# Kernel optimization log

Hardware: AMD Instinct MI355X
Metric: run time of the kernel (lower is better)

Reference implementation:

```python
import jax, jax.numpy as jnp
import numpy as np

B, S, D, H = 2, 2048, 1024, 16
DK = D // H  # 64
SCALE = DK ** (-0.5)  # NOTE: module divides by this, i.e. multiplies scores by sqrt(DK)


def setup_inputs() -> dict:
    key = jax.random.key(0)
    ks = jax.random.split(key, 9)
    std = D ** (-0.5)
    return {
        "x": jax.random.normal(ks[0], (B, S, D), dtype=jnp.float32),
        "attention_mask": jnp.ones((B, S), dtype=jnp.int32),
        "Wq": jax.random.normal(ks[1], (D, D), dtype=jnp.float32) * std,
        "bq": jnp.zeros((D,), dtype=jnp.float32),
        "Wk": jax.random.normal(ks[2], (D, D), dtype=jnp.float32) * std,
        "bk": jnp.zeros((D,), dtype=jnp.float32),
        "Wv": jax.random.normal(ks[3], (D, D), dtype=jnp.float32) * std,
        "bv": jnp.zeros((D,), dtype=jnp.float32),
        "Wo": jax.random.normal(ks[4], (D, D), dtype=jnp.float32) * std,
        "bo": jnp.zeros((D,), dtype=jnp.float32),
    }


def _split_heads(t):
    # [B, S, D] -> [B, H, S, DK]
    return t.reshape(B, S, H, DK).transpose(0, 2, 1, 3)


def reference(x, attention_mask, Wq, bq, Wk, bk, Wv, bv, Wo, bo):
    q = _split_heads(x @ Wq.T + bq)
    k = _split_heads(x @ Wk.T + bk)
    v = _split_heads(x @ Wv.T + bv)

    # faithful to source: sim = (q @ k^T) / scale with scale = dk**-0.5
    sim = jnp.einsum("bhqd,bhkd->bhqk", q, k) / SCALE

    # key-padding mask: positions where attention_mask == 0 are masked out
    neg = jnp.finfo(sim.dtype).min
    keep = attention_mask.astype(bool)[:, None, None, :]  # [B,1,1,S]
    sim = jnp.where(keep, sim, neg)

    attn = jax.nn.softmax(sim, axis=-1)  # dropout is identity at inference
    out = jnp.einsum("bhqk,bhkd->bhqd", attn, v)
    out = out.transpose(0, 2, 1, 3).reshape(B, S, D)  # merge heads
    return out @ Wo.T + bo
```

## Files before the change

kernel.cpp:

```cpp
#include <hip/hip_runtime.h>
#include <hip/hip_bf16.h>
#include <math.h>

#define BB 2
#define SS 2048
#define DD 1024
#define HH 16
#define DKK 64
#define BH (BB * HH)

typedef __bf16 bf16_t;
typedef _Float16 f16_t;
typedef __attribute__((ext_vector_type(8))) _Float16 f16x8;
typedef __attribute__((ext_vector_type(4))) _Float16 f16x4;
typedef __attribute__((ext_vector_type(4))) float f32x4;

#define GLD_LDS(gp, lp) __builtin_amdgcn_global_load_lds( \
    (const __attribute__((address_space(1))) void*)(gp),  \
    (__attribute__((address_space(3))) void*)(lp), 16, 0, 0)

__global__ void cast_x_flags(const float* __restrict__ in, f16_t* __restrict__ out,
                             const int* __restrict__ mask, int* __restrict__ flags, int n) {
    int i = blockIdx.x * blockDim.x + threadIdx.x;
    int stride = gridDim.x * blockDim.x;
    for (; i < n; i += stride) out[i] = (f16_t)in[i];
    if (blockIdx.x == 0 && threadIdx.x < BB * (SS / 128)) {
        int f = threadIdx.x;
        int b = f / (SS / 128), t = f % (SS / 128);
        const int* p = mask + b * SS + t * 128;
        int all = 1;
        for (int j = 0; j < 128; ++j) all &= (p[j] != 0);
        flags[f] = all;
    }
}

__global__ void cast_wqk(const float* __restrict__ Wq, const float* __restrict__ Wk,
                         f16_t* __restrict__ hi, f16_t* __restrict__ lo, int nw) {
    int i = blockIdx.x * blockDim.x + threadIdx.x;
    int stride = gridDim.x * blockDim.x;
    for (; i < 2 * nw; i += stride) {
        float v = (i < nw) ? Wq[i] : Wk[i - nw];
        f16_t h = (f16_t)v;
        hi[i] = h;
        lo[i] = (f16_t)(v - (float)h);
    }
}

__global__ void cast_wvo(const float* __restrict__ Wv, const float* __restrict__ Wo,
                         f16_t* __restrict__ wv, f16_t* __restrict__ wo, int nw) {
    int i = blockIdx.x * blockDim.x + threadIdx.x;
    int stride = gridDim.x * blockDim.x;
    for (; i < 2 * nw; i += stride) {
        if (i < nw) wv[i] = (f16_t)Wv[i];
        else        wo[i - nw] = (f16_t)Wo[i - nw];
    }
}

__global__ __launch_bounds__(256) void gemm_qkv(const f16_t* __restrict__ Af,
                                                const f16_t* __restrict__ Wqkh,
                                                const f16_t* __restrict__ Wqkl,
                                                const f16_t* __restrict__ Wvf,
                                                const float* __restrict__ bq,
                                                const float* __restrict__ bk,
                                                const float* __restrict__ bv,
                                                f16_t* __restrict__ q_o,
                                                f16_t* __restrict__ k_o,
                                                f16_t* __restrict__ vt_o,
                                                int K) {
    __shared__ __align__(16) f16_t sA[4096];
    __shared__ __align__(16) f16_t sB0[4096];
    __shared__ __align__(16) f16_t sB1[4096];

    const int tid  = threadIdx.x;
    const int wv   = tid >> 6;
    const int lane = tid & 63;
    const int quad = lane >> 4;
    const int l15  = lane & 15;
    const int wr   = wv >> 1;
    const int wc   = wv & 1;
    const int row0 = blockIdx.y * 128;
    const int col0 = blockIdx.x * 128;
    const bool isV = (col0 >= 2048);

    const f16_t* B0 = isV ? (Wvf + (long)(col0 - 2048) * K) : (Wqkh + (long)col0 * K);
    const f16_t* B1 = isV ? nullptr : (Wqkl + (long)col0 * K);

    f32x4 acc[4][4] = {};

    const int srow = tid >> 2;
    const int scol = (tid & 3) * 8;
    const long aoff = (long)(row0 + srow) * K + scol;
    const long boff = (long)srow * K + scol;

    if (isV) {
#pragma unroll 1
        for (int kb = 0; kb < K; kb += 32) {
#pragma unroll
            for (int p = 0; p < 2; ++p) {
                const long go = (long)p * 64 * K + kb;
                const int lo = p * 2048 + wv * 512;
                GLD_LDS(Af + aoff + go, sA + lo);
                GLD_LDS(B0 + boff + go, sB0 + lo);
            }
            __syncthreads();
            f16x8 af[4];
#pragma unroll
            for (int mt = 0; mt < 4; ++mt)
                af[mt] = *(const f16x8*)&sA[(wr * 64 + mt * 16 + l15) * 32 + quad * 8];
#pragma unroll
            for (int nt = 0; nt < 4; ++nt) {
                f16x8 b0 = *(const f16x8*)&sB0[(wc * 64 + nt * 16 + l15) * 32 + quad * 8];
#pragma unroll
                for (int mt = 0; mt < 4; ++mt)
                    acc[mt][nt] = __builtin_amdgcn_mfma_f32_16x16x32_f16(af[mt], b0, acc[mt][nt], 0, 0, 0);
            }
            __syncthreads();
        }
    } else {
#pragma unroll 1
        for (int kb = 0; kb < K; kb += 32) {
#pragma unroll
            for (int p = 0; p < 2; ++p) {
                const long go = (long)p * 64 * K + kb;
                const int lo = p * 2048 + wv * 512;
                GLD_LDS(Af + aoff + go, sA + lo);
                GLD_LDS(B0 + boff + go, sB0 + lo);
                GLD_LDS(B1 + boff + go, sB1 + lo);
            }
            __syncthreads();
            f16x8 af[4];
#pragma unroll
            for (int mt = 0; mt < 4; ++mt)
                af[mt] = *(const f16x8*)&sA[(wr * 64 + mt * 16 + l15) * 32 + quad * 8];
#pragma unroll
            for (int nt = 0; nt < 4; ++nt) {
                f16x8 b0 = *(const f16x8*)&sB0[(wc * 64 + nt * 16 + l15) * 32 + quad * 8];
                f16x8 b1 = *(const f16x8*)&sB1[(wc * 64 + nt * 16 + l15) * 32 + quad * 8];
#pragma unroll
                for (int mt = 0; mt < 4; ++mt) {
                    acc[mt][nt] = __builtin_amdgcn_mfma_f32_16x16x32_f16(af[mt], b0, acc[mt][nt], 0, 0, 0);
                    acc[mt][nt] = __builtin_amdgcn_mfma_f32_16x16x32_f16(af[mt], b1, acc[mt][nt], 0, 0, 0);
                }
            }
            __syncthreads();
        }
    }

    if (isV) {
#pragma unroll
        for (int nt = 0; nt < 4; ++nt) {
            const int colv = (col0 - 2048) + wc * 64 + nt * 16 + l15;
            const float bvv = bv[colv];
            const int hq = colv >> 6, dk = colv & 63;
#pragma unroll
            for (int mt = 0; mt < 4; ++mt) {
                const int grow0 = row0 + wr * 64 + mt * 16 + quad * 4;
                const int bq2 = grow0 >> 11;
                const int s0  = grow0 & (SS - 1);
                f16x4 pk;
#pragma unroll
                for (int r = 0; r < 4; ++r) pk[r] = (f16_t)(acc[mt][nt][r] + bvv);
                *(f16x4*)(vt_o + ((long)(bq2 * HH + hq) * DKK + dk) * SS + s0) = pk;
            }
        }
    } else {
        const bool isK = (col0 >= 1024);
        const float* bias = isK ? bk : bq;
        f16_t* op = isK ? k_o : q_o;
#pragma unroll
        for (int nt = 0; nt < 4; ++nt) {
            const int gcol = (col0 & 1023) + wc * 64 + nt * 16 + l15;
            const float bvv = bias[gcol];
            const int hq = gcol >> 6, dk = gcol & 63;
#pragma unroll
            for (int mt = 0; mt < 4; ++mt) {
                const int grow0 = row0 + wr * 64 + mt * 16 + quad * 4;
#pragma unroll
                for (int r = 0; r < 4; ++r) {
                    int grow = grow0 + r;
                    float vvv = acc[mt][nt][r] + bvv;
                    long off = (((long)(grow >> 11) * HH + hq) * SS + (grow & (SS - 1))) * DKK + dk;
                    op[off] = (f16_t)vvv;
                }
            }
        }
    }
}

__global__ __launch_bounds__(256) void gemm_o(const f16_t* __restrict__ Ah,
                                              const f16_t* __restrict__ Bhp,
                                              const float* __restrict__ bias,
                                              float* __restrict__ outf,
                                              int N, int K) {
    __shared__ __align__(16) f16_t lds[2048 + 4096];
    f16_t* Ash = lds;
    f16_t* Bsh = lds + 2048;

    const int tid  = threadIdx.x;
    const int wv   = tid >> 6;
    const int lane = tid & 63;
    const int quad = lane >> 4;
    const int l15  = lane & 15;
    const int wr   = wv >> 1;
    const int wc   = wv & 1;
    const int row0 = blockIdx.y * 64;
    const int col0 = blockIdx.x * 128;

    f32x4 acc[2][4] = {};

    const int srow = lane >> 2;
    const int scol = (lane & 3) * 8;
    const f16_t* gA  = Ah  + (long)(row0 + wv * 16 + srow) * K + scol;
    const f16_t* gB0 = Bhp + (long)(col0 + wv * 16 + srow) * K + scol;
    const f16_t* gB1 = Bhp + (long)(col0 + (wv + 4) * 16 + srow) * K + scol;
    f16_t* lA  = Ash + wv * 512;
    f16_t* lB0 = Bsh + wv * 512;
    f16_t* lB1 = Bsh + (wv + 4) * 512;

#pragma unroll 1
    for (int kb = 0; kb < K; kb += 32) {
        GLD_LDS(gA + kb, lA);
        GLD_LDS(gB0 + kb, lB0);
        GLD_LDS(gB1 + kb, lB1);
        __syncthreads();

        f16x8 af[2];
#pragma unroll
        for (int mt = 0; mt < 2; ++mt)
            af[mt] = *(const f16x8*)&Ash[(wr * 32 + mt * 16 + l15) * 32 + quad * 8];
#pragma unroll
        for (int nt = 0; nt < 4; ++nt) {
            f16x8 bh = *(const f16x8*)&Bsh[(wc * 64 + nt * 16 + l15) * 32 + quad * 8];
#pragma unroll
            for (int mt = 0; mt < 2; ++mt)
                acc[mt][nt] = __builtin_amdgcn_mfma_f32_16x16x32_f16(af[mt], bh, acc[mt][nt], 0, 0, 0);
        }
        __syncthreads();
    }

#pragma unroll
    for (int mt = 0; mt < 2; ++mt) {
#pragma unroll
        for (int nt = 0; nt < 4; ++nt) {
            const int gcol  = col0 + wc * 64 + nt * 16 + l15;
            const float bvv = bias[gcol];
            const int grow0 = row0 + wr * 32 + mt * 16 + quad * 4;
#pragma unroll
            for (int r = 0; r < 4; ++r)
                outf[(long)(grow0 + r) * N + gcol] = acc[mt][nt][r] + bvv;
        }
    }
}

__global__ __launch_bounds__(256) void attn_mfma5(const f16_t* __restrict__ Qp,
                                                  const f16_t* __restrict__ Kp,
                                                  const f16_t* __restrict__ Vtp,
                                                  const int* __restrict__ mask,
                                                  const int* __restrict__ flags,
                                                  f16_t* __restrict__ ctx,
                                                  int seq_len) {
    __shared__ __align__(16) f16_t Ksh[2][4096];
    __shared__ __align__(16) f16_t Vsh[2][4096];
    __shared__ __align__(16) f16_t Psh[4][16 * 132];

    const int tid  = threadIdx.x;
    const int wv   = tid >> 6;
    const int lane = tid & 63;
    const int quad = lane >> 4;
    const int l15  = lane & 15;
    const int bh   = blockIdx.y;
    const int b    = bh >> 4;
    const int h    = bh & 15;
    const int q0   = blockIdx.x * 64 + wv * 16;

    const long kb = (long)bh * SS * DKK;

    f16x8 qf[2];
    {
        const f16_t* pq = Qp + kb + (long)(q0 + l15) * DKK + quad * 8;
        qf[0] = *(const f16x8*)pq;
        qf[1] = *(const f16x8*)(pq + 32);
        const f16_t qs = (f16_t)(8.0f * 1.44269504088896f);
#pragma unroll
        for (int j = 0; j < 8; ++j) { qf[0][j] *= qs; qf[1][j] *= qs; }
    }

    f16x8 ones;
#pragma unroll
    for (int j = 0; j < 8; ++j) ones[j] = (f16_t)1.0f;

    f32x4 o[4], lacc;
    float m[4];
#pragma unroll
    for (int r = 0; r < 4; ++r) {
        o[r] = (f32x4){0.f, 0.f, 0.f, 0.f};
        m[r] = -1e30f;
    }
    lacc = (f32x4){0.f, 0.f, 0.f, 0.f};

    const int* mrow = mask + b * SS;
    const int* frow = flags + b * (SS / 128);

    const int srow8 = lane >> 3;
    const int gcolB = ((lane & 7) ^ srow8) * 8;

#pragma unroll 1
    for (int kt = 0; kt < seq_len; kt += 128) {
#pragma unroll
        for (int c = 0; c < 2; ++c) {
            const int kc = kt + c * 64;
#pragma unroll
            for (int p = 0; p < 2; ++p) {
                const int i = wv * 2 + p;
                const int row = i * 8 + srow8;
                GLD_LDS(Kp + kb + (long)(kc + row) * DKK + gcolB, &Ksh[c][i * 512]);
                GLD_LDS(Vtp + kb + (long)row * SS + kc + gcolB, &Vsh[c][i * 512]);
            }
        }
        __syncthreads();

        f32x4 s[8];
#pragma unroll
        for (int nt = 0; nt < 8; ++nt) s[nt] = (f32x4){0.f, 0.f, 0.f, 0.f};
#pragma unroll
        for (int nt = 0; nt < 8; ++nt) {
            const int c = nt >> 2;
            const int kr = (nt & 3) * 16 + l15;
#pragma unroll
            for (int dt = 0; dt < 2; ++dt) {
                f16x8 kf = *(const f16x8*)&Ksh[c][kr * 64 + (((dt * 4 + quad) ^ (l15 & 7)) << 3)];
                s[nt] = __builtin_amdgcn_mfma_f32_16x16x32_f16(qf[dt], kf, s[nt], 0, 0, 0);
            }
        }

        if (!frow[kt >> 7]) {
#pragma unroll
            for (int nt = 0; nt < 8; ++nt) {
                int keep = mrow[kt + nt * 16 + l15];
#pragma unroll
                for (int r = 0; r < 4; ++r)
                    s[nt][r] = keep ? s[nt][r] : -1e30f;
            }
        }

        float tm[4];
#pragma unroll
        for (int r = 0; r < 4; ++r) {
            tm[r] = fmaxf(fmaxf(fmaxf(s[0][r], s[1][r]), fmaxf(s[2][r], s[3][r])),
                          fmaxf(fmaxf(s[4][r], s[5][r]), fmaxf(s[6][r], s[7][r])));
        }
#pragma unroll
        for (int off = 1; off < 16; off <<= 1) {
#pragma unroll
            for (int r = 0; r < 4; ++r) tm[r] = fmaxf(tm[r], __shfl_xor(tm[r], off));
        }

        float alpha[4];
#pragma unroll
        for (int r = 0; r < 4; ++r) {
            float mn = fmaxf(m[r], tm[r]);
            alpha[r] = exp2f(m[r] - mn);
            m[r] = mn;
        }

#pragma unroll
        for (int nt = 0; nt < 8; ++nt) {
#pragma unroll
            for (int r = 0; r < 4; ++r) {
                float p = exp2f(s[nt][r] - m[r]);
                Psh[wv][(quad * 4 + r) * 132 + nt * 16 + l15] = (f16_t)p;
            }
        }

#pragma unroll
        for (int t = 0; t < 4; ++t)
#pragma unroll
            for (int r = 0; r < 4; ++r) o[t][r] *= alpha[r];
#pragma unroll
        for (int r = 0; r < 4; ++r) lacc[r] *= alpha[r];

#pragma unroll
        for (int kk = 0; kk < 4; ++kk) {
            const int c = kk >> 1;
            const int kk2 = kk & 1;
            f16x4 pa = *(const f16x4*)&Psh[wv][l15 * 132 + kk * 32 + quad * 8];
            f16x4 pb = *(const f16x4*)&Psh[wv][l15 * 132 + kk * 32 + quad * 8 + 4];
            f16x8 pf = __builtin_shufflevector(pa, pb, 0, 1, 2, 3, 4, 5, 6, 7);
#pragma unroll
            for (int t = 0; t < 4; ++t) {
                const int vr = t * 16 + l15;
                f16x8 vf = *(const f16x8*)&Vsh[c][vr * 64 + (((kk2 * 4 + quad) ^ (l15 & 7)) << 3)];
                o[t] = __builtin_amdgcn_mfma_f32_16x16x32_f16(pf, vf, o[t], 0, 0, 0);
            }
            lacc = __builtin_amdgcn_mfma_f32_16x16x32_f16(pf, ones, lacc, 0, 0, 0);
        }
        __syncthreads();
    }

    float inv[4];
#pragma unroll
    for (int r = 0; r < 4; ++r) inv[r] = 1.0f / lacc[r];
#pragma unroll
    for (int t = 0; t < 4; ++t) {
        int d = t * 16 + l15;
#pragma unroll
        for (int r = 0; r < 4; ++r) {
            int tok = b * SS + q0 + quad * 4 + r;
            ctx[(long)tok * DD + h * DKK + d] = (f16_t)(o[t][r] * inv[r]);
        }
    }
}

extern "C" void kernel_launch(void* const* d_in, const int* in_sizes, int n_in,
                              void* d_out, int out_size, void* d_ws, size_t ws_size,
                              hipStream_t stream) {
    const float* x  = (const float*)d_in[0];
    const int* mask = (const int*)d_in[1];
    const float* Wq = (const float*)d_in[2];
    const float* bq = (const float*)d_in[3];
    const float* Wk = (const float*)d_in[4];
    const float* bk = (const float*)d_in[5];
    const float* Wv = (const float*)d_in[6];
    const float* bv = (const float*)d_in[7];
    const float* Wo = (const float*)d_in[8];
    const float* bo = (const float*)d_in[9];
    float* out = (float*)d_out;

    const long NX = (long)BB * SS * DD;
    const long NW = (long)DD * DD;

    char* ws = (char*)d_ws;
    f16_t* xf   = (f16_t*)ws; ws += NX * 2;
    f16_t* wqkh = (f16_t*)ws; ws += 2 * NW * 2;
    f16_t* wqkl = (f16_t*)ws; ws += 2 * NW * 2;
    f16_t* wvf  = (f16_t*)ws; ws += NW * 2;
    f16_t* wof  = (f16_t*)ws; ws += NW * 2;
    f16_t* qf   = (f16_t*)ws; ws += NX * 2;
    f16_t* kf   = (f16_t*)ws; ws += NX * 2;
    f16_t* vt   = (f16_t*)ws; ws += NX * 2;
    f16_t* ctx  = (f16_t*)ws; ws += NX * 2;
    int*   flg  = (int*)ws;   ws += 64 * 4;

    cast_x_flags<<<2048, 256, 0, stream>>>(x, xf, mask, flg, (int)NX);
    cast_wqk<<<2048, 256, 0, stream>>>(Wq, Wk, wqkh, wqkl, (int)NW);
    cast_wvo<<<2048, 256, 0, stream>>>(Wv, Wo, wvf, wof, (int)NW);

    dim3 gqkv(3 * DD / 128, (BB * SS) / 128);
    gemm_qkv<<<gqkv, 256, 0, stream>>>(xf, wqkh, wqkl, wvf, bq, bk, bv, qf, kf, vt, DD);

    dim3 agrid(SS / 64, BH);
    attn_mfma5<<<agrid, 256, 0, stream>>>(qf, kf, vt, mask, flg, ctx, SS);

    dim3 go(DD / 128, (BB * SS) / 64);
    gemm_o<<<go, 256, 0, stream>>>(ctx, wof, bo, out, DD, DD);
}
```

Measured before the change: 285.5 us.

## Keep softmax probabilities in registers by computing transposed scores in attention

The QK^T MFMA now takes K as the A operand, producing S^T, so each lane holds a query column. That lets P be packed straight into registers as the A operand of a 16x16x16 MFMA for PV, with no LDS round trip for P. Row max and row sum become per-lane scalars reduced with two cross-lane shuffles, and the ones-vector MFMA for the sum is dropped. The rescale of the output accumulator is skipped when no lane's max grew. The trade-off is smaller-K MFMAs and extra shuffles to broadcast alpha and the sum.

```diff
diff --git a/kernel.cpp b/kernel.cpp
--- a/kernel.cpp
+++ b/kernel.cpp
@@ -14,10 +14,17 @@
 typedef __attribute__((ext_vector_type(8))) _Float16 f16x8;
 typedef __attribute__((ext_vector_type(4))) _Float16 f16x4;
 typedef __attribute__((ext_vector_type(4))) float f32x4;
+typedef __attribute__((ext_vector_type(4))) int i32x4;
+typedef __attribute__((ext_vector_type(2))) int i32x2;
 
 #define GLD_LDS(gp, lp) __builtin_amdgcn_global_load_lds( \
     (const __attribute__((address_space(1))) void*)(gp),  \
     (__attribute__((address_space(3))) void*)(lp), 16, 0, 0)
+
+static __device__ __forceinline__ int pkrtz(float a, float b) {
+    auto h = __builtin_amdgcn_cvt_pkrtz(a, b);
+    return __builtin_bit_cast(int, h);
+}
 
 __global__ void cast_x_flags(const float* __restrict__ in, f16_t* __restrict__ out,
                              const int* __restrict__ mask, int* __restrict__ flags, int n) {
@@ -252,7 +259,7 @@
     }
 }
 
-__global__ __launch_bounds__(256) void attn_mfma5(const f16_t* __restrict__ Qp,
+__global__ __launch_bounds__(256) void attn_mfma7(const f16_t* __restrict__ Qp,
                                                   const f16_t* __restrict__ Kp,
                                                   const f16_t* __restrict__ Vtp,
                                                   const int* __restrict__ mask,
@@ -261,7 +268,6 @@
                                                   int seq_len) {
     __shared__ __align__(16) f16_t Ksh[2][4096];
     __shared__ __align__(16) f16_t Vsh[2][4096];
-    __shared__ __align__(16) f16_t Psh[4][16 * 132];
 
     const int tid  = threadIdx.x;
     const int wv   = tid >> 6;
@@ -285,18 +291,11 @@
         for (int j = 0; j < 8; ++j) { qf[0][j] *= qs; qf[1][j] *= qs; }
     }
 
-    f16x8 ones;
-#pragma unroll
-    for (int j = 0; j < 8; ++j) ones[j] = (f16_t)1.0f;
-
-    f32x4 o[4], lacc;
-    float m[4];
-#pragma unroll
-    for (int r = 0; r < 4; ++r) {
-        o[r] = (f32x4){0.f, 0.f, 0.f, 0.f};
-        m[r] = -1e30f;
-    }
-    lacc = (f32x4){0.f, 0.f, 0.f, 0.f};
+    f32x4 o[4];
+#pragma unroll
+    for (int r = 0; r < 4; ++r) o[r] = (f32x4){0.f, 0.f, 0.f, 0.f};
+    float lsum = 0.f;
+    float m = -1e30f;
 
     const int* mrow = mask + b * SS;
     const int* frow = flags + b * (SS / 128);
@@ -329,77 +328,72 @@
 #pragma unroll
             for (int dt = 0; dt < 2; ++dt) {
                 f16x8 kf = *(const f16x8*)&Ksh[c][kr * 64 + (((dt * 4 + quad) ^ (l15 & 7)) << 3)];
-                s[nt] = __builtin_amdgcn_mfma_f32_16x16x32_f16(qf[dt], kf, s[nt], 0, 0, 0);
+                s[nt] = __builtin_amdgcn_mfma_f32_16x16x32_f16(kf, qf[dt], s[nt], 0, 0, 0);
             }
         }
 
         if (!frow[kt >> 7]) {
 #pragma unroll
             for (int nt = 0; nt < 8; ++nt) {
-                int keep = mrow[kt + nt * 16 + l15];
+                i32x4 kp = *(const i32x4*)&mrow[kt + nt * 16 + quad * 4];
 #pragma unroll
                 for (int r = 0; r < 4; ++r)
-                    s[nt][r] = keep ? s[nt][r] : -1e30f;
-            }
-        }
-
-        float tm[4];
-#pragma unroll
-        for (int r = 0; r < 4; ++r) {
-            tm[r] = fmaxf(fmaxf(fmaxf(s[0][r], s[1][r]), fmaxf(s[2][r], s[3][r])),
+                    s[nt][r] = kp[r] ? s[nt][r] : -1e30f;
+            }
+        }
+
+        f32x4 mx;
+#pragma unroll
+        for (int r = 0; r < 4; ++r)
+            mx[r] = fmaxf(fmaxf(fmaxf(s[0][r], s[1][r]), fmaxf(s[2][r], s[3][r])),
                           fmaxf(fmaxf(s[4][r], s[5][r]), fmaxf(s[6][r], s[7][r])));
-        }
-#pragma unroll
-        for (int off = 1; off < 16; off <<= 1) {
-#pragma unroll
-            for (int r = 0; r < 4; ++r) tm[r] = fmaxf(tm[r], __shfl_xor(tm[r], off));
-        }
-
-        float alpha[4];
-#pragma unroll
-        for (int r = 0; r < 4; ++r) {
-            float mn = fmaxf(m[r], tm[r]);
-            alpha[r] = exp2f(m[r] - mn);
-            m[r] = mn;
-        }
+        float tm = fmaxf(fmaxf(mx[0], mx[1]), fmaxf(mx[2], mx[3]));
+        tm = fmaxf(tm, __shfl_xor(tm, 16));
+        tm = fmaxf(tm, __shfl_xor(tm, 32));
+
+        const float mn = fmaxf(m, tm);
+        if (__any(tm > m)) {
+            const float alpha = exp2f(m - mn);
+            lsum *= alpha;
+            float a4[4];
+#pragma unroll
+            for (int r = 0; r < 4; ++r)
+                a4[r] = __shfl(alpha, quad * 4 + r);
+#pragma unroll
+            for (int t = 0; t < 4; ++t)
+#pragma unroll
+                for (int r = 0; r < 4; ++r) o[t][r] *= a4[r];
+        }
+        m = mn;
 
 #pragma unroll
         for (int nt = 0; nt < 8; ++nt) {
-#pragma unroll
-            for (int r = 0; r < 4; ++r) {
-                float p = exp2f(s[nt][r] - m[r]);
-                Psh[wv][(quad * 4 + r) * 132 + nt * 16 + l15] = (f16_t)p;
-            }
-        }
-
-#pragma unroll
-        for (int t = 0; t < 4; ++t)
-#pragma unroll
-            for (int r = 0; r < 4; ++r) o[t][r] *= alpha[r];
-#pragma unroll
-        for (int r = 0; r < 4; ++r) lacc[r] *= alpha[r];
-
-#pragma unroll
-        for (int kk = 0; kk < 4; ++kk) {
-            const int c = kk >> 1;
-            const int kk2 = kk & 1;
-            f16x4 pa = *(const f16x4*)&Psh[wv][l15 * 132 + kk * 32 + quad * 8];
-            f16x4 pb = *(const f16x4*)&Psh[wv][l15 * 132 + kk * 32 + quad * 8 + 4];
-            f16x8 pf = __builtin_shufflevector(pa, pb, 0, 1, 2, 3, 4, 5, 6, 7);
+            const int c = nt >> 2;
+            float p0 = exp2f(s[nt][0] - mn);
+            float p1 = exp2f(s[nt][1] - mn);
+            float p2 = exp2f(s[nt][2] - mn);
+            float p3 = exp2f(s[nt][3] - mn);
+            lsum += (p0 + p1) + (p2 + p3);
+            i32x2 pp;
+            pp[0] = pkrtz(p0, p1);
+            pp[1] = pkrtz(p2, p3);
+            f16x4 paf = __builtin_bit_cast(f16x4, pp);
+            const int vcol = ((((nt & 3) * 2 + (quad >> 1)) ^ (l15 & 7)) << 3) + ((quad & 1) << 2);
 #pragma unroll
             for (int t = 0; t < 4; ++t) {
-                const int vr = t * 16 + l15;
-                f16x8 vf = *(const f16x8*)&Vsh[c][vr * 64 + (((kk2 * 4 + quad) ^ (l15 & 7)) << 3)];
-                o[t] = __builtin_amdgcn_mfma_f32_16x16x32_f16(pf, vf, o[t], 0, 0, 0);
-            }
-            lacc = __builtin_amdgcn_mfma_f32_16x16x32_f16(pf, ones, lacc, 0, 0, 0);
+                f16x4 vB = *(const f16x4*)&Vsh[c][(t * 16 + l15) * 64 + vcol];
+                o[t] = __builtin_amdgcn_mfma_f32_16x16x16f16(paf, vB, o[t], 0, 0, 0);
+            }
         }
         __syncthreads();
     }
 
+    lsum += __shfl_xor(lsum, 16);
+    lsum += __shfl_xor(lsum, 32);
     float inv[4];
 #pragma unroll
-    for (int r = 0; r < 4; ++r) inv[r] = 1.0f / lacc[r];
+    for (int r = 0; r < 4; ++r)
+        inv[r] = 1.0f / __shfl(lsum, quad * 4 + r);
 #pragma unroll
     for (int t = 0; t < 4; ++t) {
         int d = t * 16 + l15;
@@ -449,7 +443,7 @@
     gemm_qkv<<<gqkv, 256, 0, stream>>>(xf, wqkh, wqkl, wvf, bq, bk, bv, qf, kf, vt, DD);
 
     dim3 agrid(SS / 64, BH);
-    attn_mfma5<<<agrid, 256, 0, stream>>>(qf, kf, vt, mask, flg, ctx, SS);
+    attn_mfma7<<<agrid, 256, 0, stream>>>(qf, kf, vt, mask, flg, ctx, SS);
 
     dim3 go(DD / 128, (BB * SS) / 64);
     gemm_o<<<go, 256, 0, stream>>>(ctx, wof, bo, out, DD, DD);
```

After: 284.7 us. About the same (-0.3%).
